# Kernel tuning notes

Hardware: AMD Instinct MI355X
Metric: run time of the kernel (lower is better)

Reference implementation:

```python
import jax, jax.numpy as jnp
import numpy as np

N = 10000   # nodes
E = 40000   # edges
B = 250     # graphs (40 nodes each)
NODE_IN = 74
EDGE_IN = 12
H = 64      # hidden_feats
RD = 1024   # readout_feats


def setup_inputs() -> dict:
    key = jax.random.key(0)
    ks = jax.random.split(key, 32)
    w = lambda i, shape: jax.random.normal(ks[i], shape, jnp.float32) * 0.05
    inp = {
        'node_attr': jax.random.normal(ks[0], (N, NODE_IN), jnp.float32),
        'edge_attr': jax.random.normal(ks[1], (E, EDGE_IN), jnp.float32),
        'src': jax.random.randint(ks[2], (E,), 0, N, jnp.int32),
        'dst': jax.random.randint(ks[3], (E,), 0, N, jnp.int32),
        'graph_ids': (jnp.arange(N, dtype=jnp.int32) // (N // B)),
        'num_graphs': B,
        # project_node_feats: Linear(NODE_IN, H)
        'Wp': w(4, (H, NODE_IN)), 'bp': w(5, (H,)),
        # FALayer gate: Linear(2H, 1)
        'Wg': w(6, (1, 2 * H)), 'bg': w(7, (1,)),
        # edge_network: Linear(EDGE_IN + 1, H*H)
        'We': w(8, (H * H, EDGE_IN + 1)), 'be': w(9, (H * H,)),
        'nnconv_bias': w(10, (H,)),
        # GRU(H, H), single layer
        'gru_wih': w(11, (3 * H, H)), 'gru_whh': w(12, (3 * H, H)),
        'gru_bih': w(13, (3 * H,)), 'gru_bhh': w(14, (3 * H,)),
        # Set2Set LSTM: input 4H -> hidden 2H
        'lstm_wih': w(15, (8 * H, 4 * H)), 'lstm_whh': w(16, (8 * H, 2 * H)),
        'lstm_bih': w(17, (8 * H,)), 'lstm_bhh': w(18, (8 * H,)),
        # sparsify: Linear(4H, RD) + PReLU
        'Ws': w(19, (RD, 4 * H)), 'bs': w(20, (RD,)),
        'prelu_a': jnp.asarray(0.25, jnp.float32),
    }
    return inp


def _seg_softmax(e, ids, num):
    m = jax.ops.segment_max(e, ids, num_segments=num)
    ex = jnp.exp(e - m[ids])
    den = jax.ops.segment_sum(ex, ids, num_segments=num)
    return ex / den[ids]


def _forward(node_attr, edge_attr, src, dst, graph_ids, num_graphs,
             Wp, bp, Wg, bg, We, be, nnconv_bias,
             gru_wih, gru_whh, gru_bih, gru_bhh,
             lstm_wih, lstm_whh, lstm_bih, lstm_bhh,
             Ws, bs, prelu_a):
    n = node_attr.shape[0]
    h0 = jax.nn.relu(node_attr @ Wp.T + bp)            # (N, H)

    # FALayer (eval mode: dropout is identity)
    deg = jax.ops.segment_sum(jnp.ones(src.shape[0], node_attr.dtype), dst,
                              num_segments=n)           # in-degrees (N,)
    h2 = jnp.concatenate([h0[dst], h0[src]], axis=1)    # (E, 2H)
    t = jnp.tanh(h2 @ Wg.T + bg)[:, 0]                  # (E,)
    e_gate = 0.3 + t * deg[dst] * deg[src]              # (E,)
    efeat = jnp.concatenate([edge_attr, e_gate[:, None]], axis=-1)  # (E, EDGE_IN+1)

    # NNConv per-edge dynamic weights (edge_feats fixed across steps)
    W_edge = (efeat @ We.T + be).reshape(-1, H, H)      # (E, H, H)

    h = h0
    hid = h0  # GRU hidden state
    for _ in range(3):  # num_step_message_passing
        m = jnp.einsum('ei,eio->eo', h[src], W_edge)    # per-edge matvec
        agg = jax.ops.segment_sum(m, dst, num_segments=n) + nnconv_bias
        x = jax.nn.relu(agg)
        # torch GRU (gate order r, z, n)
        gi = x @ gru_wih.T + gru_bih
        gh = hid @ gru_whh.T + gru_bhh
        r = jax.nn.sigmoid(gi[:, :H] + gh[:, :H])
        z = jax.nn.sigmoid(gi[:, H:2 * H] + gh[:, H:2 * H])
        ng = jnp.tanh(gi[:, 2 * H:] + r * gh[:, 2 * H:])
        hid = (1.0 - z) * ng + z * hid
        h = hid

    feat = jnp.concatenate([h0, h], axis=1)             # (N, 2H)
    D = 2 * H

    # Set2Set readout (LSTM gate order i, f, g, o)
    q_star = jnp.zeros((num_graphs, 2 * D), feat.dtype)
    hl = jnp.zeros((num_graphs, D), feat.dtype)
    cl = jnp.zeros((num_graphs, D), feat.dtype)
    for _ in range(3):  # num_step_set2set
        g4 = q_star @ lstm_wih.T + lstm_bih + hl @ lstm_whh.T + lstm_bhh
        i = jax.nn.sigmoid(g4[:, :D])
        f = jax.nn.sigmoid(g4[:, D:2 * D])
        gg = jnp.tanh(g4[:, 2 * D:3 * D])
        o = jax.nn.sigmoid(g4[:, 3 * D:])
        cl = f * cl + i * gg
        hl = o * jnp.tanh(cl)
        q = hl                                           # (B, D)
        sc = jnp.sum(feat * q[graph_ids], axis=-1)       # (N,)
        alpha = _seg_softmax(sc, graph_ids, num_graphs)
        readout = jax.ops.segment_sum(feat * alpha[:, None], graph_ids,
                                      num_segments=num_graphs)  # (B, D)
        q_star = jnp.concatenate([q, readout], axis=-1)  # (B, 2D)

    out = q_star @ Ws.T + bs
    return jnp.where(out >= 0, out, prelu_a * out)       # PReLU


def reference(node_attr, edge_attr, src, dst, graph_ids, num_graphs,
              Wp, bp, Wg, bg, We, be, nnconv_bias,
              gru_wih, gru_whh, gru_bih, gru_bhh,
              lstm_wih, lstm_whh, lstm_bih, lstm_bhh,
              Ws, bs, prelu_a):
    return _forward(node_attr, edge_attr, src, dst, graph_ids, num_graphs,
                    Wp, bp, Wg, bg, We, be, nnconv_bias,
                    gru_wih, gru_whh, gru_bih, gru_bhh,
                    lstm_wih, lstm_whh, lstm_bih, lstm_bhh,
                    Ws, bs, prelu_a)
```

## Files before the change

kernel.cpp:

```cpp
#include <hip/hip_runtime.h>
#include <math.h>


#define H 64
#define NODE_IN 74
#define EDGE_IN 12
#define EF 14
#define GCAP 256
#define MGH 1088

__device__ __forceinline__ float sigmoidf(float x) {
    return 1.0f / (1.0f + expf(-x));
}

template<int AOP, int EOP>
__global__ __launch_bounds__(256)
void gemm_k(const float* __restrict__ A, int lda,
            const float* __restrict__ B, int ldb,
            float* __restrict__ C, int ldc,
            int M, int N, int K,
            const float* __restrict__ abias,
            const float* __restrict__ cbias,
            const float* __restrict__ prelu_a)
{
    __shared__ float sA[64][68];
    __shared__ float sB[64][68];

    const int tid = threadIdx.x;
    const int bm  = blockIdx.x * 64;
    const int bn  = blockIdx.y * 64;
    const int tx  = tid & 15;
    const int ty  = tid >> 4;

    float acc[4][4] = {{0.f}};

    for (int k0 = 0; k0 < K; k0 += 64) {
        #pragma unroll
        for (int t = 0; t < 4; ++t) {
            int idx = tid + t * 256;
            int r   = idx >> 4;
            int c   = (idx & 15) << 2;
            float4 v = {0.f, 0.f, 0.f, 0.f};
            int gm = bm + r;
            if (gm < M) {
                v = *reinterpret_cast<const float4*>(A + (size_t)gm * lda + (k0 + c));
                if (AOP == 1) {
                    v.x = fmaxf(v.x + abias[k0 + c + 0], 0.f);
                    v.y = fmaxf(v.y + abias[k0 + c + 1], 0.f);
                    v.z = fmaxf(v.z + abias[k0 + c + 2], 0.f);
                    v.w = fmaxf(v.w + abias[k0 + c + 3], 0.f);
                }
            }
            sA[c + 0][r] = v.x;
            sA[c + 1][r] = v.y;
            sA[c + 2][r] = v.z;
            sA[c + 3][r] = v.w;
        }
        #pragma unroll
        for (int t = 0; t < 4; ++t) {
            int idx = tid + t * 256;
            int r   = idx >> 4;
            int c   = (idx & 15) << 2;
            float4 v = *reinterpret_cast<const float4*>(B + (size_t)(k0 + r) * ldb + (bn + c));
            *reinterpret_cast<float4*>(&sB[r][c]) = v;
        }
        __syncthreads();

        #pragma unroll
        for (int kk = 0; kk < 64; ++kk) {
            float4 av = *reinterpret_cast<const float4*>(&sA[kk][ty * 4]);
            float4 bv = *reinterpret_cast<const float4*>(&sB[kk][tx * 4]);
            float a0 = av.x, a1 = av.y, a2 = av.z, a3 = av.w;
            float b0 = bv.x, b1 = bv.y, b2 = bv.z, b3 = bv.w;
            acc[0][0] = fmaf(a0, b0, acc[0][0]); acc[0][1] = fmaf(a0, b1, acc[0][1]);
            acc[0][2] = fmaf(a0, b2, acc[0][2]); acc[0][3] = fmaf(a0, b3, acc[0][3]);
            acc[1][0] = fmaf(a1, b0, acc[1][0]); acc[1][1] = fmaf(a1, b1, acc[1][1]);
            acc[1][2] = fmaf(a1, b2, acc[1][2]); acc[1][3] = fmaf(a1, b3, acc[1][3]);
            acc[2][0] = fmaf(a2, b0, acc[2][0]); acc[2][1] = fmaf(a2, b1, acc[2][1]);
            acc[2][2] = fmaf(a2, b2, acc[2][2]); acc[2][3] = fmaf(a2, b3, acc[2][3]);
            acc[3][0] = fmaf(a3, b0, acc[3][0]); acc[3][1] = fmaf(a3, b1, acc[3][1]);
            acc[3][2] = fmaf(a3, b2, acc[3][2]); acc[3][3] = fmaf(a3, b3, acc[3][3]);
        }
        __syncthreads();
    }

    float pa = (EOP == 1) ? prelu_a[0] : 0.f;
    #pragma unroll
    for (int i = 0; i < 4; ++i) {
        int gm = bm + ty * 4 + i;
        if (gm < M) {
            float4 v;
            float* vv = reinterpret_cast<float*>(&v);
            #pragma unroll
            for (int j = 0; j < 4; ++j) {
                float c = acc[i][j];
                if (EOP == 1) {
                    c += cbias[bn + tx * 4 + j];
                    c = (c >= 0.f) ? c : pa * c;
                }
                vv[j] = c;
            }
            *reinterpret_cast<float4*>(C + (size_t)gm * ldc + bn + tx * 4) = v;
        }
    }
}

__global__ __launch_bounds__(256)
void prep_all_k(const float* __restrict__ na, const float* __restrict__ Wp,
                const float* __restrict__ bp, float* __restrict__ h0,
                const float* __restrict__ We, const float* __restrict__ be,
                const float* __restrict__ wih, const float* __restrict__ whh,
                const float* __restrict__ lwih, const float* __restrict__ lwhh,
                const float* __restrict__ Ws,
                float* __restrict__ We2b, float* __restrict__ wihT,
                float* __restrict__ WlT, float* __restrict__ WsT,
                const int* __restrict__ dst, float* __restrict__ deg,
                const int* __restrict__ gid, int* __restrict__ gcnt,
                int* __restrict__ glist,
                int N, int E,
                int nb_h0, int nb_prep, int nb_deg)
{
    int b   = blockIdx.x;
    int tid = threadIdx.x;
    if (b < nb_h0) {
        int idx = b * 256 + tid;
        if (idx >= N * H) return;
        int n = idx >> 6, o = idx & 63;
        const float* x = na + (size_t)n * NODE_IN;
        const float* w = Wp + (size_t)o * NODE_IN;
        float acc = bp[o];
        #pragma unroll
        for (int k = 0; k < NODE_IN; ++k) acc = fmaf(x[k], w[k], acc);
        h0[idx] = fmaxf(acc, 0.f);
    } else if (b < nb_h0 + nb_prep) {
        int t = (b - nb_h0) * 256 + tid;
        if (t < 69632) {
            int i = t / MGH, j = t % MGH;
            float v;
            if (j < 896) {
                int k = j >> 6, o = j & 63;
                v = (k < 13) ? We[(size_t)(i * 64 + o) * 13 + k] : be[i * 64 + o];
            } else {
                int jj = j - 896;
                v = whh[(size_t)jj * 64 + i];
            }
            We2b[t] = v;
        } else if (t < 81920) {
            int u = t - 69632;
            int i = u / 192, j = u % 192;
            wihT[u] = wih[(size_t)j * 64 + i];
        } else if (t < 278528) {
            int u = t - 81920;
            int k = u >> 9, j = u & 511;
            WlT[u] = (k < 256) ? lwih[(size_t)j * 256 + k]
                               : lwhh[(size_t)j * 128 + (k - 256)];
        } else if (t < 540672) {
            int u = t - 278528;
            int k = u >> 10, j = u & 1023;
            WsT[u] = Ws[(size_t)j * 256 + k];
        }
    } else if (b < nb_h0 + nb_prep + nb_deg) {
        int e = (b - nb_h0 - nb_prep) * 256 + tid;
        if (e < E) atomicAdd(&deg[dst[e]], 1.0f);
    } else {
        int n = (b - nb_h0 - nb_prep - nb_deg) * 256 + tid;
        if (n < N) {
            int g = gid[n];
            int p = atomicAdd(&gcnt[g], 1);
            if (p < GCAP) glist[(size_t)g * GCAP + p] = n;
        }
    }
}

__global__ __launch_bounds__(256)
void gate_k(const float* __restrict__ h0, const float* __restrict__ ea,
            const int* __restrict__ src, const int* __restrict__ dst,
            const float* __restrict__ Wg, const float* __restrict__ bg,
            const float* __restrict__ deg, float* __restrict__ ef, int E)
{
    int e    = blockIdx.x * 4 + (threadIdx.x >> 6);
    int lane = threadIdx.x & 63;
    if (e >= E) return;
    int s = src[e], d = dst[e];
    float v = Wg[lane]      * h0[(size_t)d * H + lane]
            + Wg[H + lane]  * h0[(size_t)s * H + lane];
    #pragma unroll
    for (int off = 32; off; off >>= 1) v += __shfl_xor(v, off);
    if (lane < EF) {
        float out;
        if (lane < EDGE_IN) out = ea[(size_t)e * EDGE_IN + lane];
        else if (lane == EDGE_IN) {
            float t = tanhf(v + bg[0]);
            out = 0.3f + t * deg[d] * deg[s];
        } else out = 1.0f;
        ef[(size_t)e * EF + lane] = out;
    }
}

__global__ __launch_bounds__(256)
void edge_k(const float* __restrict__ M, const float* __restrict__ ef,
            const int* __restrict__ src, const int* __restrict__ dst,
            float* __restrict__ agg, int E)
{
    int e = blockIdx.x * 4 + (threadIdx.x >> 6);
    int o = threadIdx.x & 63;
    if (e >= E) return;
    int s = src[e], d = dst[e];
    const float* Ms = M + (size_t)s * MGH;
    const float* f  = ef + (size_t)e * EF;
    float m = 0.f;
    #pragma unroll
    for (int k = 0; k < EF; ++k) m = fmaf(f[k], Ms[k * H + o], m);
    atomicAdd(&agg[(size_t)d * H + o], m);
}

__global__ __launch_bounds__(256)
void gru_k(const float* __restrict__ gi, const float* __restrict__ gh, int ghld,
           const float* __restrict__ bih, const float* __restrict__ bhh,
           const float* __restrict__ hin, float* __restrict__ hout,
           float* __restrict__ agg, int N)
{
    int idx = blockIdx.x * 256 + threadIdx.x;
    if (idx >= N * H) return;
    int n = idx >> 6, o = idx & 63;
    const float* gin = gi + (size_t)n * 192;
    const float* ghn = gh + (size_t)n * ghld;
    float r  = sigmoidf(gin[o]       + bih[o]       + ghn[o]       + bhh[o]);
    float z  = sigmoidf(gin[64 + o]  + bih[64 + o]  + ghn[64 + o]  + bhh[64 + o]);
    float gn = ghn[128 + o] + bhh[128 + o];
    float ng = tanhf(gin[128 + o] + bih[128 + o] + r * gn);
    float hv = hin[idx];
    hout[idx] = (1.f - z) * ng + z * hv;
    agg[idx]  = 0.f;
}

__global__ __launch_bounds__(64)
void att_k(const float* __restrict__ h0, const float* __restrict__ h,
           const float* __restrict__ g4,
           const float* __restrict__ lbih, const float* __restrict__ lbhh,
           float* __restrict__ cl,
           const int* __restrict__ glist, const int* __restrict__ gcnt,
           float* __restrict__ Acat)
{
    int b    = blockIdx.x;
    int lane = threadIdx.x;
    __shared__ float q[128];
    __shared__ float sc[GCAP];

    const float* g = g4 + (size_t)b * 512;
    #pragma unroll
    for (int t = 0; t < 2; ++t) {
        int d = lane + t * 64;
        float ii = sigmoidf(g[d]       + lbih[d]       + lbhh[d]);
        float ff = sigmoidf(g[128 + d] + lbih[128 + d] + lbhh[128 + d]);
        float gg = tanhf  (g[256 + d] + lbih[256 + d] + lbhh[256 + d]);
        float oo = sigmoidf(g[384 + d] + lbih[384 + d] + lbhh[384 + d]);
        float c  = ff * cl[(size_t)b * 128 + d] + ii * gg;
        cl[(size_t)b * 128 + d] = c;
        q[d] = oo * tanhf(c);
    }
    __syncthreads();

    int c = gcnt[b]; if (c > GCAP) c = GCAP;

    float lmax = -INFINITY;
    for (int i = lane; i < c; i += 64) {
        int n = glist[(size_t)b * GCAP + i];
        const float* f0 = h0 + (size_t)n * H;
        const float* f1 = h  + (size_t)n * H;
        float s = 0.f;
        #pragma unroll
        for (int j = 0; j < H; ++j) s = fmaf(f0[j], q[j], s);
        #pragma unroll
        for (int j = 0; j < H; ++j) s = fmaf(f1[j], q[H + j], s);
        sc[i] = s;
        lmax = fmaxf(lmax, s);
    }
    #pragma unroll
    for (int off = 32; off; off >>= 1) lmax = fmaxf(lmax, __shfl_xor(lmax, off));

    float lsum = 0.f;
    for (int i = lane; i < c; i += 64) {
        float e = expf(sc[i] - lmax);
        sc[i] = e;
        lsum += e;
    }
    #pragma unroll
    for (int off = 32; off; off >>= 1) lsum += __shfl_xor(lsum, off);
    __syncthreads();

    float inv = 1.f / lsum;
    float r0 = 0.f, r1 = 0.f;
    for (int i = 0; i < c; ++i) {
        int n = glist[(size_t)b * GCAP + i];
        float w = sc[i];
        r0 = fmaf(w, h0[(size_t)n * H + lane], r0);
        r1 = fmaf(w, h [(size_t)n * H + lane], r1);
    }
    float* A = Acat + (size_t)b * 384;
    A[lane]       = q[lane];
    A[64 + lane]  = q[64 + lane];
    A[128 + lane] = r0 * inv;
    A[192 + lane] = r1 * inv;
    A[256 + lane] = q[lane];
    A[320 + lane] = q[64 + lane];
}

extern "C" void kernel_launch(void* const* d_in, const int* in_sizes, int n_in,
                              void* d_out, int out_size, void* d_ws, size_t ws_size,
                              hipStream_t stream)
{
    (void)n_in; (void)ws_size;
    const float* node_attr = (const float*)d_in[0];
    const float* edge_attr = (const float*)d_in[1];
    const int*   src       = (const int*)d_in[2];
    const int*   dst       = (const int*)d_in[3];
    const int*   gid       = (const int*)d_in[4];
    const float* Wp        = (const float*)d_in[6];
    const float* bp        = (const float*)d_in[7];
    const float* Wg        = (const float*)d_in[8];
    const float* bg        = (const float*)d_in[9];
    const float* We        = (const float*)d_in[10];
    const float* be        = (const float*)d_in[11];
    const float* nb        = (const float*)d_in[12];
    const float* gwih      = (const float*)d_in[13];
    const float* gwhh      = (const float*)d_in[14];
    const float* gbih      = (const float*)d_in[15];
    const float* gbhh      = (const float*)d_in[16];
    const float* lwih      = (const float*)d_in[17];
    const float* lwhh      = (const float*)d_in[18];
    const float* lbih      = (const float*)d_in[19];
    const float* lbhh      = (const float*)d_in[20];
    const float* Ws        = (const float*)d_in[21];
    const float* bs        = (const float*)d_in[22];
    const float* pa        = (const float*)d_in[23];

    const int N = in_sizes[0] / NODE_IN;
    const int E = in_sizes[2];
    const int B = out_size / 1024;

    float* ws = (float*)d_ws;
    size_t off = 0;
    auto alloc = [&](size_t n) { size_t o = off; off += (n + 63) & ~(size_t)63; return o; };
    size_t oDEG  = alloc(N);
    size_t oCL   = alloc((size_t)B * 128);
    size_t oACAT = alloc((size_t)B * 384);
    size_t oGCNT = alloc(B);
    size_t oAGG  = alloc((size_t)N * H);
    size_t zero_beg = oDEG, zero_end = off;
    size_t oH0   = alloc((size_t)N * H);
    size_t oHB   = alloc((size_t)N * H);
    size_t oEF   = alloc((size_t)E * EF);
    size_t oGL   = alloc((size_t)B * GCAP);
    size_t oWE2  = alloc(64 * MGH);
    size_t oWIHT = alloc(64 * 192);
    size_t oWLT  = alloc(384 * 512);
    size_t oWST  = alloc(256 * 1024);
    size_t oG4   = alloc((size_t)B * 512);
    size_t oGI   = alloc((size_t)N * 192);
    size_t oM    = alloc((size_t)N * MGH);

    float* deg  = ws + oDEG;
    float* clb  = ws + oCL;
    float* Acat = ws + oACAT;
    int*   gcnt = (int*)(ws + oGCNT);
    float* agg  = ws + oAGG;
    float* h0   = ws + oH0;
    float* hbuf = ws + oHB;
    float* ef   = ws + oEF;
    int*   glist= (int*)(ws + oGL);
    float* We2b = ws + oWE2;
    float* wihT = ws + oWIHT;
    float* WlT  = ws + oWLT;
    float* WsT  = ws + oWST;
    float* g4   = ws + oG4;
    float* gib  = ws + oGI;
    float* Mb   = ws + oM;
    float* ghb  = Mb + 896;

    const int mt = (N + 63) / 64;
    const int bt = (B + 63) / 64;

    hipMemsetAsync(ws + zero_beg, 0, (zero_end - zero_beg) * sizeof(float), stream);
    const int nb_h0   = (N * H + 255) / 256;
    const int nb_prep = (540672 + 255) / 256;
    const int nb_deg  = (E + 255) / 256;
    const int nb_gl   = (N + 255) / 256;
    prep_all_k<<<nb_h0 + nb_prep + nb_deg + nb_gl, 256, 0, stream>>>(
        node_attr, Wp, bp, h0, We, be, gwih, gwhh, lwih, lwhh, Ws,
        We2b, wihT, WlT, WsT, dst, deg, gid, gcnt, glist,
        N, E, nb_h0, nb_prep, nb_deg);
    gate_k<<<(E + 3) / 4, 256, 0, stream>>>(h0, edge_attr, src, dst, Wg, bg, deg, ef, E);

    const float* hcur = h0;
    for (int step = 0; step < 3; ++step) {
        gemm_k<0, 0><<<dim3(mt, MGH / 64), 256, 0, stream>>>(
            hcur, H, We2b, MGH, Mb, MGH, N, MGH, 64, nullptr, nullptr, nullptr);
        edge_k<<<(E + 3) / 4, 256, 0, stream>>>(Mb, ef, src, dst, agg, E);
        gemm_k<1, 0><<<dim3(mt, 3), 256, 0, stream>>>(agg, H, wihT, 192, gib, 192,
                                                      N, 192, 64, nb, nullptr, nullptr);
        gru_k<<<(N * H + 255) / 256, 256, 0, stream>>>(gib, ghb, MGH, gbih, gbhh,
                                                       hcur, hbuf, agg, N);
        hcur = hbuf;
    }

    for (int s = 0; s < 3; ++s) {
        gemm_k<0, 0><<<dim3(bt, 8), 256, 0, stream>>>(Acat, 384, WlT, 512, g4, 512,
                                                      B, 512, 384, nullptr, nullptr, nullptr);
        att_k<<<B, 64, 0, stream>>>(h0, hbuf, g4, lbih, lbhh, clb, glist, gcnt, Acat);
    }

    gemm_k<0, 1><<<dim3(bt, 16), 256, 0, stream>>>(Acat, 384, WsT, 1024, (float*)d_out, 1024,
                                                   B, 1024, 256, nullptr, bs, pa);
}
```

Baseline: 432.7 us.

## Replace atomic edge scatter with CSR gather aggregation and 128-row GEMM tiles

Builds a dst-sorted CSR of edges once: per-node in-degree counts, a single-block prefix scan and cursor-based edge placement inside the gate kernel. Each NNConv step then gathers messages per destination node with no float atomics, which also removes the need to re-zero agg in the GRU kernel. Separately, the large node GEMMs now use a 128x64 tile with 8x4 per-thread accumulators, giving more reuse per shared-memory load. The costs are a serial single-block scan, load imbalance across nodes of different in-degree, and higher register use in the bigger GEMM tile.

Result: slower. 474.4 us (+9.6%).

```diff
diff --git a/kernel.cpp b/kernel.cpp
--- a/kernel.cpp
+++ b/kernel.cpp
@@ -13,30 +13,28 @@
     return 1.0f / (1.0f + expf(-x));
 }
 
-template<int AOP, int EOP>
+template<int AOP>
 __global__ __launch_bounds__(256)
-void gemm_k(const float* __restrict__ A, int lda,
-            const float* __restrict__ B, int ldb,
-            float* __restrict__ C, int ldc,
-            int M, int N, int K,
-            const float* __restrict__ abias,
-            const float* __restrict__ cbias,
-            const float* __restrict__ prelu_a)
-{
-    __shared__ float sA[64][68];
+void gemm128_k(const float* __restrict__ A, int lda,
+               const float* __restrict__ B, int ldb,
+               float* __restrict__ C, int ldc,
+               int M, int N, int K,
+               const float* __restrict__ abias)
+{
+    __shared__ float sA[64][132];
     __shared__ float sB[64][68];
 
     const int tid = threadIdx.x;
-    const int bm  = blockIdx.x * 64;
+    const int bm  = blockIdx.x * 128;
     const int bn  = blockIdx.y * 64;
     const int tx  = tid & 15;
     const int ty  = tid >> 4;
 
-    float acc[4][4] = {{0.f}};
+    float acc[8][4] = {{0.f}};
 
     for (int k0 = 0; k0 < K; k0 += 64) {
         #pragma unroll
-        for (int t = 0; t < 4; ++t) {
+        for (int t = 0; t < 8; ++t) {
             int idx = tid + t * 256;
             int r   = idx >> 4;
             int c   = (idx & 15) << 2;
@@ -61,8 +59,79 @@
             int idx = tid + t * 256;
             int r   = idx >> 4;
             int c   = (idx & 15) << 2;
-            float4 v = *reinterpret_cast<const float4*>(B + (size_t)(k0 + r) * ldb + (bn + c));
-            *reinterpret_cast<float4*>(&sB[r][c]) = v;
+            *reinterpret_cast<float4*>(&sB[r][c]) =
+                *reinterpret_cast<const float4*>(B + (size_t)(k0 + r) * ldb + (bn + c));
+        }
+        __syncthreads();
+
+        #pragma unroll
+        for (int kk = 0; kk < 64; ++kk) {
+            float4 a0 = *reinterpret_cast<const float4*>(&sA[kk][ty * 8]);
+            float4 a1 = *reinterpret_cast<const float4*>(&sA[kk][ty * 8 + 4]);
+            float4 bv = *reinterpret_cast<const float4*>(&sB[kk][tx * 4]);
+            float ar[8] = {a0.x, a0.y, a0.z, a0.w, a1.x, a1.y, a1.z, a1.w};
+            float br[4] = {bv.x, bv.y, bv.z, bv.w};
+            #pragma unroll
+            for (int i = 0; i < 8; ++i)
+                #pragma unroll
+                for (int j = 0; j < 4; ++j)
+                    acc[i][j] = fmaf(ar[i], br[j], acc[i][j]);
+        }
+        __syncthreads();
+    }
+
+    #pragma unroll
+    for (int i = 0; i < 8; ++i) {
+        int gm = bm + ty * 8 + i;
+        if (gm < M) {
+            float4 v = {acc[i][0], acc[i][1], acc[i][2], acc[i][3]};
+            *reinterpret_cast<float4*>(C + (size_t)gm * ldc + bn + tx * 4) = v;
+        }
+    }
+}
+
+template<int EOP>
+__global__ __launch_bounds__(256)
+void gemm_k(const float* __restrict__ A, int lda,
+            const float* __restrict__ B, int ldb,
+            float* __restrict__ C, int ldc,
+            int M, int N, int K,
+            const float* __restrict__ cbias,
+            const float* __restrict__ prelu_a)
+{
+    __shared__ float sA[64][68];
+    __shared__ float sB[64][68];
+
+    const int tid = threadIdx.x;
+    const int bm  = blockIdx.x * 64;
+    const int bn  = blockIdx.y * 64;
+    const int tx  = tid & 15;
+    const int ty  = tid >> 4;
+
+    float acc[4][4] = {{0.f}};
+
+    for (int k0 = 0; k0 < K; k0 += 64) {
+        #pragma unroll
+        for (int t = 0; t < 4; ++t) {
+            int idx = tid + t * 256;
+            int r   = idx >> 4;
+            int c   = (idx & 15) << 2;
+            float4 v = {0.f, 0.f, 0.f, 0.f};
+            int gm = bm + r;
+            if (gm < M)
+                v = *reinterpret_cast<const float4*>(A + (size_t)gm * lda + (k0 + c));
+            sA[c + 0][r] = v.x;
+            sA[c + 1][r] = v.y;
+            sA[c + 2][r] = v.z;
+            sA[c + 3][r] = v.w;
+        }
+        #pragma unroll
+        for (int t = 0; t < 4; ++t) {
+            int idx = tid + t * 256;
+            int r   = idx >> 4;
+            int c   = (idx & 15) << 2;
+            *reinterpret_cast<float4*>(&sB[r][c]) =
+                *reinterpret_cast<const float4*>(B + (size_t)(k0 + r) * ldb + (bn + c));
         }
         __syncthreads();
 
@@ -70,16 +139,13 @@
         for (int kk = 0; kk < 64; ++kk) {
             float4 av = *reinterpret_cast<const float4*>(&sA[kk][ty * 4]);
             float4 bv = *reinterpret_cast<const float4*>(&sB[kk][tx * 4]);
-            float a0 = av.x, a1 = av.y, a2 = av.z, a3 = av.w;
-            float b0 = bv.x, b1 = bv.y, b2 = bv.z, b3 = bv.w;
-            acc[0][0] = fmaf(a0, b0, acc[0][0]); acc[0][1] = fmaf(a0, b1, acc[0][1]);
-            acc[0][2] = fmaf(a0, b2, acc[0][2]); acc[0][3] = fmaf(a0, b3, acc[0][3]);
-            acc[1][0] = fmaf(a1, b0, acc[1][0]); acc[1][1] = fmaf(a1, b1, acc[1][1]);
-            acc[1][2] = fmaf(a1, b2, acc[1][2]); acc[1][3] = fmaf(a1, b3, acc[1][3]);
-            acc[2][0] = fmaf(a2, b0, acc[2][0]); acc[2][1] = fmaf(a2, b1, acc[2][1]);
-            acc[2][2] = fmaf(a2, b2, acc[2][2]); acc[2][3] = fmaf(a2, b3, acc[2][3]);
-            acc[3][0] = fmaf(a3, b0, acc[3][0]); acc[3][1] = fmaf(a3, b1, acc[3][1]);
-            acc[3][2] = fmaf(a3, b2, acc[3][2]); acc[3][3] = fmaf(a3, b3, acc[3][3]);
+            float ar[4] = {av.x, av.y, av.z, av.w};
+            float br[4] = {bv.x, bv.y, bv.z, bv.w};
+            #pragma unroll
+            for (int i = 0; i < 4; ++i)
+                #pragma unroll
+                for (int j = 0; j < 4; ++j)
+                    acc[i][j] = fmaf(ar[i], br[j], acc[i][j]);
         }
         __syncthreads();
     }
@@ -115,6 +181,7 @@
                 float* __restrict__ We2b, float* __restrict__ wihT,
                 float* __restrict__ WlT, float* __restrict__ WsT,
                 const int* __restrict__ dst, float* __restrict__ deg,
+                int* __restrict__ icnt,
                 const int* __restrict__ gid, int* __restrict__ gcnt,
                 int* __restrict__ glist,
                 int N, int E,
@@ -161,7 +228,11 @@
         }
     } else if (b < nb_h0 + nb_prep + nb_deg) {
         int e = (b - nb_h0 - nb_prep) * 256 + tid;
-        if (e < E) atomicAdd(&deg[dst[e]], 1.0f);
+        if (e < E) {
+            int d = dst[e];
+            atomicAdd(&deg[d], 1.0f);
+            atomicAdd(&icnt[d], 1);
+        }
     } else {
         int n = (b - nb_h0 - nb_prep - nb_deg) * 256 + tid;
         if (n < N) {
@@ -172,11 +243,40 @@
     }
 }
 
+__global__ __launch_bounds__(1024)
+void scan_k(const int* __restrict__ icnt, int* __restrict__ row_ptr,
+            int* __restrict__ cursor, int N)
+{
+    __shared__ int s[1024];
+    __shared__ int carry;
+    int tid = threadIdx.x;
+    if (tid == 0) { carry = 0; row_ptr[0] = 0; }
+    __syncthreads();
+    for (int base = 0; base < N; base += 1024) {
+        int i = base + tid;
+        int v = (i < N) ? icnt[i] : 0;
+        s[tid] = v;
+        __syncthreads();
+        for (int off = 1; off < 1024; off <<= 1) {
+            int t = (tid >= off) ? s[tid - off] : 0;
+            __syncthreads();
+            s[tid] += t;
+            __syncthreads();
+        }
+        int incl = s[tid] + carry;
+        if (i < N) { row_ptr[i + 1] = incl; cursor[i] = incl - v; }
+        __syncthreads();
+        if (tid == 1023) carry = incl;
+        __syncthreads();
+    }
+}
+
 __global__ __launch_bounds__(256)
 void gate_k(const float* __restrict__ h0, const float* __restrict__ ea,
             const int* __restrict__ src, const int* __restrict__ dst,
             const float* __restrict__ Wg, const float* __restrict__ bg,
-            const float* __restrict__ deg, float* __restrict__ ef, int E)
+            const float* __restrict__ deg, float* __restrict__ ef,
+            int* __restrict__ cursor, int* __restrict__ csr_eid, int E)
 {
     int e    = blockIdx.x * 4 + (threadIdx.x >> 6);
     int lane = threadIdx.x & 63;
@@ -194,31 +294,37 @@
             out = 0.3f + t * deg[d] * deg[s];
         } else out = 1.0f;
         ef[(size_t)e * EF + lane] = out;
+    } else if (lane == EF) {
+        int pos = atomicAdd(&cursor[d], 1);
+        csr_eid[pos] = e;
     }
 }
 
 __global__ __launch_bounds__(256)
-void edge_k(const float* __restrict__ M, const float* __restrict__ ef,
-            const int* __restrict__ src, const int* __restrict__ dst,
-            float* __restrict__ agg, int E)
-{
-    int e = blockIdx.x * 4 + (threadIdx.x >> 6);
-    int o = threadIdx.x & 63;
-    if (e >= E) return;
-    int s = src[e], d = dst[e];
-    const float* Ms = M + (size_t)s * MGH;
-    const float* f  = ef + (size_t)e * EF;
-    float m = 0.f;
-    #pragma unroll
-    for (int k = 0; k < EF; ++k) m = fmaf(f[k], Ms[k * H + o], m);
-    atomicAdd(&agg[(size_t)d * H + o], m);
+void agg_csr_k(const float* __restrict__ M, const float* __restrict__ ef,
+               const int* __restrict__ src, const int* __restrict__ csr_eid,
+               const int* __restrict__ row_ptr, float* __restrict__ agg, int N)
+{
+    int n    = blockIdx.x * 4 + (threadIdx.x >> 6);
+    int lane = threadIdx.x & 63;
+    if (n >= N) return;
+    int p0 = row_ptr[n], p1 = row_ptr[n + 1];
+    float a = 0.f;
+    for (int p = p0; p < p1; ++p) {
+        int e = csr_eid[p];
+        int s = src[e];
+        const float* Ms = M + (size_t)s * MGH + lane;
+        const float* f  = ef + (size_t)e * EF;
+        #pragma unroll
+        for (int k = 0; k < EF; ++k) a = fmaf(f[k], Ms[k * H], a);
+    }
+    agg[(size_t)n * H + lane] = a;
 }
 
 __global__ __launch_bounds__(256)
 void gru_k(const float* __restrict__ gi, const float* __restrict__ gh, int ghld,
            const float* __restrict__ bih, const float* __restrict__ bhh,
-           const float* __restrict__ hin, float* __restrict__ hout,
-           float* __restrict__ agg, int N)
+           const float* __restrict__ hin, float* __restrict__ hout, int N)
 {
     int idx = blockIdx.x * 256 + threadIdx.x;
     if (idx >= N * H) return;
@@ -231,7 +337,6 @@
     float ng = tanhf(gin[128 + o] + bih[128 + o] + r * gn);
     float hv = hin[idx];
     hout[idx] = (1.f - z) * ng + z * hv;
-    agg[idx]  = 0.f;
 }
 
 __global__ __launch_bounds__(64)
@@ -343,11 +448,15 @@
     size_t off = 0;
     auto alloc = [&](size_t n) { size_t o = off; off += (n + 63) & ~(size_t)63; return o; };
     size_t oDEG  = alloc(N);
+    size_t oICNT = alloc(N);
     size_t oCL   = alloc((size_t)B * 128);
     size_t oACAT = alloc((size_t)B * 384);
     size_t oGCNT = alloc(B);
+    size_t zero_beg = oDEG, zero_end = off;
+    size_t oRP   = alloc(N + 1);
+    size_t oCUR  = alloc(N);
+    size_t oCSR  = alloc(E);
     size_t oAGG  = alloc((size_t)N * H);
-    size_t zero_beg = oDEG, zero_end = off;
     size_t oH0   = alloc((size_t)N * H);
     size_t oHB   = alloc((size_t)N * H);
     size_t oEF   = alloc((size_t)E * EF);
@@ -360,26 +469,30 @@
     size_t oGI   = alloc((size_t)N * 192);
     size_t oM    = alloc((size_t)N * MGH);
 
-    float* deg  = ws + oDEG;
-    float* clb  = ws + oCL;
-    float* Acat = ws + oACAT;
-    int*   gcnt = (int*)(ws + oGCNT);
-    float* agg  = ws + oAGG;
-    float* h0   = ws + oH0;
-    float* hbuf = ws + oHB;
-    float* ef   = ws + oEF;
-    int*   glist= (int*)(ws + oGL);
-    float* We2b = ws + oWE2;
-    float* wihT = ws + oWIHT;
-    float* WlT  = ws + oWLT;
-    float* WsT  = ws + oWST;
-    float* g4   = ws + oG4;
-    float* gib  = ws + oGI;
-    float* Mb   = ws + oM;
-    float* ghb  = Mb + 896;
-
-    const int mt = (N + 63) / 64;
-    const int bt = (B + 63) / 64;
+    float* deg   = ws + oDEG;
+    int*   icnt  = (int*)(ws + oICNT);
+    float* clb   = ws + oCL;
+    float* Acat  = ws + oACAT;
+    int*   gcnt  = (int*)(ws + oGCNT);
+    int*   rowp  = (int*)(ws + oRP);
+    int*   cursor= (int*)(ws + oCUR);
+    int*   csr   = (int*)(ws + oCSR);
+    float* agg   = ws + oAGG;
+    float* h0    = ws + oH0;
+    float* hbuf  = ws + oHB;
+    float* ef    = ws + oEF;
+    int*   glist = (int*)(ws + oGL);
+    float* We2b  = ws + oWE2;
+    float* wihT  = ws + oWIHT;
+    float* WlT   = ws + oWLT;
+    float* WsT   = ws + oWST;
+    float* g4    = ws + oG4;
+    float* gib   = ws + oGI;
+    float* Mb    = ws + oM;
+    float* ghb   = Mb + 896;
+
+    const int mt128 = (N + 127) / 128;
+    const int bt    = (B + 63) / 64;
 
     hipMemsetAsync(ws + zero_beg, 0, (zero_end - zero_beg) * sizeof(float), stream);
     const int nb_h0   = (N * H + 255) / 256;
@@ -388,28 +501,30 @@
     const int nb_gl   = (N + 255) / 256;
     prep_all_k<<<nb_h0 + nb_prep + nb_deg + nb_gl, 256, 0, stream>>>(
         node_attr, Wp, bp, h0, We, be, gwih, gwhh, lwih, lwhh, Ws,
-        We2b, wihT, WlT, WsT, dst, deg, gid, gcnt, glist,
+        We2b, wihT, WlT, WsT, dst, deg, icnt, gid, gcnt, glist,
         N, E, nb_h0, nb_prep, nb_deg);
-    gate_k<<<(E + 3) / 4, 256, 0, stream>>>(h0, edge_attr, src, dst, Wg, bg, deg, ef, E);
+    scan_k<<<1, 1024, 0, stream>>>(icnt, rowp, cursor, N);
+    gate_k<<<(E + 3) / 4, 256, 0, stream>>>(h0, edge_attr, src, dst, Wg, bg, deg,
+                                            ef, cursor, csr, E);
 
     const float* hcur = h0;
     for (int step = 0; step < 3; ++step) {
-        gemm_k<0, 0><<<dim3(mt, MGH / 64), 256, 0, stream>>>(
-            hcur, H, We2b, MGH, Mb, MGH, N, MGH, 64, nullptr, nullptr, nullptr);
-        edge_k<<<(E + 3) / 4, 256, 0, stream>>>(Mb, ef, src, dst, agg, E);
-        gemm_k<1, 0><<<dim3(mt, 3), 256, 0, stream>>>(agg, H, wihT, 192, gib, 192,
-                                                      N, 192, 64, nb, nullptr, nullptr);
+        gemm128_k<0><<<dim3(mt128, MGH / 64), 256, 0, stream>>>(
+            hcur, H, We2b, MGH, Mb, MGH, N, MGH, 64, nullptr);
+        agg_csr_k<<<(N + 3) / 4, 256, 0, stream>>>(Mb, ef, src, csr, rowp, agg, N);
+        gemm128_k<1><<<dim3(mt128, 3), 256, 0, stream>>>(
+            agg, H, wihT, 192, gib, 192, N, 192, 64, nb);
         gru_k<<<(N * H + 255) / 256, 256, 0, stream>>>(gib, ghb, MGH, gbih, gbhh,
-                                                       hcur, hbuf, agg, N);
+                                                       hcur, hbuf, N);
         hcur = hbuf;
     }
 
     for (int s = 0; s < 3; ++s) {
-        gemm_k<0, 0><<<dim3(bt, 8), 256, 0, stream>>>(Acat, 384, WlT, 512, g4, 512,
-                                                      B, 512, 384, nullptr, nullptr, nullptr);
+        gemm_k<0><<<dim3(bt, 8), 256, 0, stream>>>(Acat, 384, WlT, 512, g4, 512,
+                                                   B, 512, 384, nullptr, nullptr);
         att_k<<<B, 64, 0, stream>>>(h0, hbuf, g4, lbih, lbhh, clb, glist, gcnt, Acat);
     }
 
-    gemm_k<0, 1><<<dim3(bt, 16), 256, 0, stream>>>(Acat, 384, WsT, 1024, (float*)d_out, 1024,
-                                                   B, 1024, 256, nullptr, bs, pa);
-}
+    gemm_k<1><<<dim3(bt, 16), 256, 0, stream>>>(Acat, 384, WsT, 1024, (float*)d_out, 1024,
+                                                B, 1024, 256, bs, pa);
+}
```
